# Performance work log

Hardware: AMD Instinct MI355X
Metric: run time of the kernel (lower is better)

The kernel has to match this reference:

```python
import jax, jax.numpy as jnp
import numpy as np

EPS = 1e-7  # keras.backend.epsilon()

def setup_inputs() -> dict:
    key = jax.random.key(0)
    x = jax.random.normal(key, (2000000, 20), dtype=jnp.float32)
    return {"x": x}

def reference(x) -> jnp.ndarray:
    # [B, 20] -> [B, 2, 10]; normalize each length-10 segment by its mean and
    # population std (tf.math.reduce_std uses ddof=0), then add epsilon to std.
    xr = jnp.reshape(x, (-1, 2, 10))
    mean = jnp.mean(xr, axis=-1, keepdims=True)
    var = jnp.mean(jnp.square(xr - mean), axis=-1, keepdims=True)
    std = jnp.sqrt(var)
    return (xr - mean) / (std + EPS)
```

## Files before the change

kernel.cpp:

```cpp
#include <hip/hip_runtime.h>


constexpr float EPS = 1e-7f;
constexpr int THREADS = 256;
constexpr int ROWS_PER_BLOCK = 256;
constexpr int LDS_STRIDE = 21;

__global__ __launch_bounds__(256) void stdz_kernel(const float* __restrict__ x,
                                                   float* __restrict__ out,
                                                   int nrows) {
    __shared__ float tile[ROWS_PER_BLOCK * LDS_STRIDE];

    const int t = threadIdx.x;
    const long long block_row0 = (long long)blockIdx.x * ROWS_PER_BLOCK;
    const long long total_f4 = (long long)nrows * 5;
    const long long base_f4 = block_row0 * 5;

    const float4* __restrict__ xin4 = reinterpret_cast<const float4*>(x);

#pragma unroll
    for (int k = 0; k < 5; ++k) {
        long long g = base_f4 + (long long)(k * THREADS + t);
        if (g < total_f4) {
            float4 v = xin4[g];
            int idx = k * THREADS + t;
            int r = idx / 5;
            int c = idx % 5;
            float* p = &tile[r * LDS_STRIDE + c * 4];
            p[0] = v.x; p[1] = v.y; p[2] = v.z; p[3] = v.w;
        }
    }
    __syncthreads();

    {
        long long row = block_row0 + t;
        if (row < nrows) {
            float* rp = &tile[t * LDS_STRIDE];
            float v[20];
#pragma unroll
            for (int j = 0; j < 20; ++j) v[j] = rp[j];

#pragma unroll
            for (int s = 0; s < 2; ++s) {
                float sum = 0.0f;
#pragma unroll
                for (int j = 0; j < 10; ++j) sum += v[s * 10 + j];
                float mean = sum * 0.1f;

                float var = 0.0f;
#pragma unroll
                for (int j = 0; j < 10; ++j) {
                    float d = v[s * 10 + j] - mean;
                    var += d * d;
                }
                float inv = 1.0f / (sqrtf(var * 0.1f) + EPS);

#pragma unroll
                for (int j = 0; j < 10; ++j) v[s * 10 + j] = (v[s * 10 + j] - mean) * inv;
            }

#pragma unroll
            for (int j = 0; j < 20; ++j) rp[j] = v[j];
        }
    }
    __syncthreads();

    float4* __restrict__ o4 = reinterpret_cast<float4*>(out);
#pragma unroll
    for (int k = 0; k < 5; ++k) {
        long long g = base_f4 + (long long)(k * THREADS + t);
        if (g < total_f4) {
            int idx = k * THREADS + t;
            int r = idx / 5;
            int c = idx % 5;
            const float* p = &tile[r * LDS_STRIDE + c * 4];
            o4[g] = make_float4(p[0], p[1], p[2], p[3]);
        }
    }
}

extern "C" void kernel_launch(void* const* d_in, const int* in_sizes, int n_in,
                              void* d_out, int out_size, void* d_ws, size_t ws_size,
                              hipStream_t stream) {
    const float* x = (const float*)d_in[0];
    float* out = (float*)d_out;
    int nrows = in_sizes[0] / 20;
    int blocks = (nrows + ROWS_PER_BLOCK - 1) / ROWS_PER_BLOCK;
    stdz_kernel<<<blocks, THREADS, 0, stream>>>(x, out, nrows);
}
```

Before: 62.04 us.

## Partition LDS tile per wave, use wave barriers and nontemporal stores

```diff
diff --git a/kernel.cpp b/kernel.cpp
--- a/kernel.cpp
+++ b/kernel.cpp
@@ -3,39 +3,48 @@
 
 constexpr float EPS = 1e-7f;
 constexpr int THREADS = 256;
-constexpr int ROWS_PER_BLOCK = 256;
+constexpr int ROWS_PER_WAVE = 64;
+constexpr int WAVES_PER_BLOCK = 4;
+constexpr int ROWS_PER_BLOCK = ROWS_PER_WAVE * WAVES_PER_BLOCK;
 constexpr int LDS_STRIDE = 21;
+
+typedef float f32x4 __attribute__((ext_vector_type(4)));
 
 __global__ __launch_bounds__(256) void stdz_kernel(const float* __restrict__ x,
                                                    float* __restrict__ out,
                                                    int nrows) {
-    __shared__ float tile[ROWS_PER_BLOCK * LDS_STRIDE];
+    __shared__ float tile[WAVES_PER_BLOCK][ROWS_PER_WAVE * LDS_STRIDE];
 
-    const int t = threadIdx.x;
-    const long long block_row0 = (long long)blockIdx.x * ROWS_PER_BLOCK;
+    const int wave = threadIdx.x >> 6;
+    const int lane = threadIdx.x & 63;
+    float* __restrict__ wt = tile[wave];
+
+    const long long wave_row0 =
+        (long long)blockIdx.x * ROWS_PER_BLOCK + (long long)wave * ROWS_PER_WAVE;
     const long long total_f4 = (long long)nrows * 5;
-    const long long base_f4 = block_row0 * 5;
+    const long long base_f4 = wave_row0 * 5;
 
-    const float4* __restrict__ xin4 = reinterpret_cast<const float4*>(x);
+    const f32x4* __restrict__ xin4 = reinterpret_cast<const f32x4*>(x);
 
 #pragma unroll
     for (int k = 0; k < 5; ++k) {
-        long long g = base_f4 + (long long)(k * THREADS + t);
+        long long g = base_f4 + (long long)(k * ROWS_PER_WAVE + lane);
         if (g < total_f4) {
-            float4 v = xin4[g];
-            int idx = k * THREADS + t;
+            f32x4 v = xin4[g];
+            int idx = k * ROWS_PER_WAVE + lane;
             int r = idx / 5;
-            int c = idx % 5;
-            float* p = &tile[r * LDS_STRIDE + c * 4];
+            int c = idx - 5 * r;
+            float* p = &wt[r * LDS_STRIDE + c * 4];
             p[0] = v.x; p[1] = v.y; p[2] = v.z; p[3] = v.w;
         }
     }
-    __syncthreads();
+    asm volatile("s_waitcnt lgkmcnt(0)" ::: "memory");
+    __builtin_amdgcn_wave_barrier();
 
     {
-        long long row = block_row0 + t;
+        long long row = wave_row0 + lane;
         if (row < nrows) {
-            float* rp = &tile[t * LDS_STRIDE];
+            float* rp = &wt[lane * LDS_STRIDE];
             float v[20];
 #pragma unroll
             for (int j = 0; j < 20; ++j) v[j] = rp[j];
@@ -63,18 +72,20 @@
             for (int j = 0; j < 20; ++j) rp[j] = v[j];
         }
     }
-    __syncthreads();
+    asm volatile("s_waitcnt lgkmcnt(0)" ::: "memory");
+    __builtin_amdgcn_wave_barrier();
 
-    float4* __restrict__ o4 = reinterpret_cast<float4*>(out);
+    f32x4* __restrict__ o4 = reinterpret_cast<f32x4*>(out);
 #pragma unroll
     for (int k = 0; k < 5; ++k) {
-        long long g = base_f4 + (long long)(k * THREADS + t);
+        long long g = base_f4 + (long long)(k * ROWS_PER_WAVE + lane);
         if (g < total_f4) {
-            int idx = k * THREADS + t;
+            int idx = k * ROWS_PER_WAVE + lane;
             int r = idx / 5;
-            int c = idx % 5;
-            const float* p = &tile[r * LDS_STRIDE + c * 4];
-            o4[g] = make_float4(p[0], p[1], p[2], p[3]);
+            int c = idx - 5 * r;
+            const float* p = &wt[r * LDS_STRIDE + c * 4];
+            f32x4 v = {p[0], p[1], p[2], p[3]};
+            __builtin_nontemporal_store(v, &o4[g]);
         }
     }
 }
```

Result: faster. 52.04 us (-16.1%).
